# Performance work log

Measured on AMD Instinct MI355X. Metric: run time of the kernel, lower is better.

Reference implementation:

```python
import jax, jax.numpy as jnp
import numpy as np

B, S, D_IN, D_MODEL, H = 2, 2048, 1024, 1024, 16
HD = D_MODEL // H


def setup_inputs() -> dict:
    key = jax.random.key(0)
    ks = jax.random.split(key, 5)
    x = jax.random.normal(ks[0], (B, S, D_IN), dtype=jnp.float32)
    # nn.Linear default init scale ~ 1/sqrt(fan_in)
    w_qkv = jax.random.normal(ks[1], (D_IN, 3 * D_MODEL), dtype=jnp.float32) / np.sqrt(D_IN)
    b_qkv = jax.random.normal(ks[2], (3 * D_MODEL,), dtype=jnp.float32) * 0.02
    w_out = jax.random.normal(ks[3], (D_MODEL, D_MODEL), dtype=jnp.float32) / np.sqrt(D_MODEL)
    b_out = jax.random.normal(ks[4], (D_MODEL,), dtype=jnp.float32) * 0.02
    return {"x": x, "w_qkv": w_qkv, "b_qkv": b_qkv, "w_out": w_out, "b_out": b_out}


def reference(x, w_qkv, b_qkv, w_out, b_out):
    b, s, _ = x.shape
    qkv = x @ w_qkv + b_qkv                       # [b, s, 3*d_model]
    # per-head layout is [q_h | k_h | v_h]: reshape to (b, s, h, 3, hd)
    qkv = qkv.reshape(b, s, H, 3, HD).transpose(0, 2, 1, 3, 4)  # [b, h, s, 3, hd]
    q, k, v = qkv[..., 0, :], qkv[..., 1, :], qkv[..., 2, :]     # each [b, h, s, hd]
    scale = 1.0 / np.sqrt(HD).astype(np.float32)
    scores = jnp.einsum('bhqd,bhkd->bhqk', q, k) * scale         # [b, h, s, s]
    causal = jnp.tril(jnp.ones((s, s), dtype=bool))              # True = keep
    scores = jnp.where(causal, scores, -jnp.inf)
    attn = jax.nn.softmax(scores, axis=-1)
    out = jnp.einsum('bhqk,bhkd->bhqd', attn, v)                 # [b, h, s, hd]
    concat = out.transpose(0, 2, 1, 3).reshape(b, s, D_MODEL)
    return concat @ w_out + b_out
```

## Files before the change

kernel.cpp:

```cpp
#include <hip/hip_runtime.h>
#include <hip/hip_bf16.h>
#include <stdint.h>

typedef __attribute__((ext_vector_type(8))) short bf16x8;
typedef __attribute__((ext_vector_type(4))) float f32x4;

#define DEVFN static __device__ __forceinline__

typedef const __attribute__((address_space(1))) void* gas_ptr;
typedef __attribute__((address_space(3))) void* las_ptr;

DEVFN void async16(const void* g, void* l) {
  __builtin_amdgcn_global_load_lds((gas_ptr)g, (las_ptr)l, 16, 0, 0);
}

#define S_LEN 2048
#define NH    16
#define HDIM  64
#define KDIM  1024
#define NQKV  3072
#define MTOK  4096

#define QK_SCALE 0.1803368801111244f

__global__ __launch_bounds__(256) void prep_kernel(
    const float* __restrict__ x, const float* __restrict__ w_qkv,
    const float* __restrict__ w_out, __hip_bfloat16* __restrict__ xb,
    __hip_bfloat16* __restrict__ wqkt, __hip_bfloat16* __restrict__ wot) {
  __shared__ float T[64][65];
  const int j = blockIdx.x;
  const int tid = threadIdx.x;
  if (j < 2048) {
    const int i = (j * 256 + tid) * 8;
    float4 a = *(const float4*)(x + i);
    float4 b = *(const float4*)(x + i + 4);
    alignas(16) __hip_bfloat16 t[8] = {
        __float2bfloat16(a.x), __float2bfloat16(a.y),
        __float2bfloat16(a.z), __float2bfloat16(a.w),
        __float2bfloat16(b.x), __float2bfloat16(b.y),
        __float2bfloat16(b.z), __float2bfloat16(b.w)};
    *(uint4*)(xb + i) = *(const uint4*)t;
    return;
  }
  const float* in;
  __hip_bfloat16* out;
  int N, n0, k0;
  if (j < 2816) {
    const int j2 = j - 2048;
    in = w_qkv; out = wqkt; N = NQKV;
    n0 = (j2 % 48) * 64; k0 = (j2 / 48) * 64;
  } else {
    const int j3 = j - 2816;
    in = w_out; out = wot; N = KDIM;
    n0 = (j3 % 16) * 64; k0 = (j3 / 16) * 64;
  }
#pragma unroll
  for (int it = 0; it < 4; it++) {
    int r = it * 16 + (tid >> 4);
    int c = (tid & 15) * 4;
    float4 v = *(const float4*)&in[(size_t)(k0 + r) * N + n0 + c];
    T[r][c + 0] = v.x; T[r][c + 1] = v.y; T[r][c + 2] = v.z; T[r][c + 3] = v.w;
  }
  __syncthreads();
#pragma unroll
  for (int it = 0; it < 4; it++) {
    int rn = it * 16 + (tid >> 4);
    int ck = (tid & 15) * 4;
    alignas(8) __hip_bfloat16 t4[4];
#pragma unroll
    for (int jj = 0; jj < 4; jj++) t4[jj] = __float2bfloat16(T[ck + jj][rn]);
    *(ushort4*)&out[(size_t)(n0 + rn) * KDIM + k0 + ck] = *(const ushort4*)t4;
  }
}

__global__ __launch_bounds__(256, 2) void qkv_gemm_kernel(
    const __hip_bfloat16* __restrict__ A,
    const __hip_bfloat16* __restrict__ Bt,
    const float* __restrict__ bias,
    __hip_bfloat16* __restrict__ qo,
    __hip_bfloat16* __restrict__ ko,
    __hip_bfloat16* __restrict__ vto) {
  __shared__ __hip_bfloat16 As[128 * 32];
  __shared__ __hip_bfloat16 Bs[128 * 32];
  __shared__ __hip_bfloat16 Tb[4][16 * 72];
  const int tid = threadIdx.x;
  const int wave = tid >> 6, lane = tid & 63;
  const int L = lane & 15, quad = lane >> 4;
  const int wm = wave >> 1, wn = wave & 1;
  const int m0 = blockIdx.y * 128, n0 = blockIdx.x * 128;

  f32x4 acc[4][4] = {};

  const int srow = tid >> 2;
  const int scol = (tid & 3) * 8;
  const __hip_bfloat16* ag = A + (size_t)(m0 + srow) * KDIM + scol;
  const __hip_bfloat16* bg = Bt + (size_t)(n0 + srow) * KDIM + scol;
  char* asd = (char*)As + wave * 1024;
  char* bsd = (char*)Bs + wave * 1024;

  for (int kt = 0; kt < KDIM; kt += 32) {
    async16(ag + kt, asd);
    async16(ag + kt + (size_t)64 * KDIM, asd + 4096);
    async16(bg + kt, bsd);
    async16(bg + kt + (size_t)64 * KDIM, bsd + 4096);
    __syncthreads();
    bf16x8 af[4], bf[4];
#pragma unroll
    for (int r = 0; r < 4; r++)
      af[r] = *(const bf16x8*)&As[(wm * 64 + r * 16 + L) * 32 + quad * 8];
#pragma unroll
    for (int c = 0; c < 4; c++)
      bf[c] = *(const bf16x8*)&Bs[(wn * 64 + c * 16 + L) * 32 + quad * 8];
#pragma unroll
    for (int r = 0; r < 4; r++)
#pragma unroll
      for (int c = 0; c < 4; c++)
        acc[r][c] = __builtin_amdgcn_mfma_f32_16x16x32_bf16(af[r], bf[c],
                                                            acc[r][c], 0, 0, 0);
    __syncthreads();
  }

  const int mbase = m0 + wm * 64;
  const int nbase = n0 + wn * 64;
  const int h = nbase / 192;
  const int t = (nbase % 192) / 64;
  const int b = mbase >> 11;
  const int s0 = mbase & 2047;
  __hip_bfloat16* Tw = &Tb[wave][0];
  float bv[4];
#pragma unroll
  for (int c = 0; c < 4; c++) bv[c] = bias[nbase + c * 16 + L];

  if (t == 2) {
#pragma unroll
    for (int c = 0; c < 4; c++) {
#pragma unroll
      for (int r = 0; r < 4; r++) {
        alignas(8) __hip_bfloat16 t4[4];
#pragma unroll
        for (int g = 0; g < 4; g++)
          t4[g] = __float2bfloat16(acc[r][c][g] + bv[c]);
        *(ushort4*)&Tw[L * 72 + r * 16 + quad * 4] = *(const ushort4*)t4;
      }
      __asm__ volatile("s_waitcnt lgkmcnt(0)" ::: "memory");
#pragma unroll
      for (int it = 0; it < 2; it++) {
        const int rr = it * 8 + (lane >> 3);
        const int cc = (lane & 7) * 8;
        uint4 u = *(const uint4*)&Tw[rr * 72 + cc];
        *(uint4*)&vto[((size_t)((b * NH + h) * HDIM + c * 16 + rr)) * S_LEN +
                      s0 + cc] = u;
      }
    }
  } else {
    __hip_bfloat16* dst = (t == 0) ? qo : ko;
    const float sc = (t == 0) ? QK_SCALE : 1.0f;
#pragma unroll
    for (int r = 0; r < 4; r++) {
#pragma unroll
      for (int c = 0; c < 4; c++)
#pragma unroll
        for (int g = 0; g < 4; g++)
          Tw[(quad * 4 + g) * 72 + c * 16 + L] =
              __float2bfloat16((acc[r][c][g] + bv[c]) * sc);
      __asm__ volatile("s_waitcnt lgkmcnt(0)" ::: "memory");
#pragma unroll
      for (int it = 0; it < 2; it++) {
        const int rr = it * 8 + (lane >> 3);
        const int cc = (lane & 7) * 8;
        uint4 u = *(const uint4*)&Tw[rr * 72 + cc];
        *(uint4*)&dst[((size_t)((b * NH + h) * S_LEN) + s0 + r * 16 + rr) *
                          HDIM + cc] = u;
      }
    }
  }
}

__global__ __launch_bounds__(256, 2) void flash_attn_kernel(
    const __hip_bfloat16* __restrict__ q,
    const __hip_bfloat16* __restrict__ k,
    const __hip_bfloat16* __restrict__ vt,
    __hip_bfloat16* __restrict__ attn) {
  __shared__ __hip_bfloat16 Ps[4][16 * 72];
  const int tid = threadIdx.x;
  const int wave = tid >> 6, lane = tid & 63;
  const int L = lane & 15, quad = lane >> 4;

  const int j = blockIdx.x;
  const int half = j >> 8;
  const int idx = j & 255;
  const int bh = idx >> 3;
  const int p = idx & 7;
  const int qi = half ? p : (15 - p);
  const int qb = qi * 128;

  const __hip_bfloat16* Qg = q + (size_t)bh * S_LEN * HDIM;
  const __hip_bfloat16* Kg = k + (size_t)bh * S_LEN * HDIM;
  const __hip_bfloat16* Vg = vt + (size_t)bh * HDIM * S_LEN;

  int wq[2];
  wq[0] = qb + wave * 16;
  wq[1] = qb + 64 + wave * 16;

  bf16x8 qf[2][2];
#pragma unroll
  for (int r = 0; r < 2; r++)
#pragma unroll
    for (int kd = 0; kd < 2; kd++)
      qf[r][kd] =
          *(const bf16x8*)&Qg[(size_t)(wq[r] + L) * HDIM + kd * 32 + quad * 8];

  float l_i[2] = {0.f, 0.f};
  f32x4 o[2][4] = {};

  bf16x8 kc[4][2], kn[4][2];
#pragma unroll
  for (int ks = 0; ks < 4; ks++)
#pragma unroll
    for (int kd = 0; kd < 2; kd++)
      kc[ks][kd] =
          *(const bf16x8*)&Kg[(size_t)(ks * 16 + L) * HDIM + kd * 32 + quad * 8];

  const int nkt = 2 * (qi + 1);
  for (int kt = 0; kt < nkt; kt++) {
    const int k0 = kt * 64;
    bf16x8 vfr[4][2];
#pragma unroll
    for (int dsb = 0; dsb < 4; dsb++)
#pragma unroll
      for (int kf = 0; kf < 2; kf++)
        vfr[dsb][kf] = *(const bf16x8*)&Vg[(size_t)(dsb * 16 + L) * S_LEN + k0 +
                                           kf * 32 + quad * 8];

    f32x4 st[2][4] = {};
#pragma unroll
    for (int r = 0; r < 2; r++)
#pragma unroll
      for (int ks = 0; ks < 4; ks++)
#pragma unroll
        for (int kd = 0; kd < 2; kd++)
          st[r][ks] = __builtin_amdgcn_mfma_f32_16x16x32_bf16(
              kc[ks][kd], qf[r][kd], st[r][ks], 0, 0, 0);

    if (kt + 1 < nkt) {
      const int k1 = k0 + 64;
#pragma unroll
      for (int ks = 0; ks < 4; ks++)
#pragma unroll
        for (int kd = 0; kd < 2; kd++)
          kn[ks][kd] = *(const bf16x8*)&Kg[(size_t)(k1 + ks * 16 + L) * HDIM +
                                           kd * 32 + quad * 8];
    }

#pragma unroll
    for (int r = 0; r < 2; r++) {
      if (k0 > wq[r] + 15) continue;
      const int qrow = wq[r] + L;
      if (k0 + 63 > wq[r]) {
#pragma unroll
        for (int ks = 0; ks < 4; ks++)
#pragma unroll
          for (int g = 0; g < 4; g++) {
            int kk = k0 + ks * 16 + quad * 4 + g;
            if (kk > qrow) st[r][ks][g] = -1e30f;
          }
      }
      float rs = 0.f;
#pragma unroll
      for (int ks = 0; ks < 4; ks++) {
        f32x4 pv;
#pragma unroll
        for (int g = 0; g < 4; g++) {
          pv[g] = __builtin_amdgcn_exp2f(st[r][ks][g]);
          rs += pv[g];
        }
        alignas(8) __hip_bfloat16 t4[4];
#pragma unroll
        for (int g = 0; g < 4; g++) t4[g] = __float2bfloat16(pv[g]);
        *(ushort4*)&Ps[wave][L * 72 + ks * 16 + quad * 4] = *(const ushort4*)t4;
      }
      l_i[r] += rs;
      __asm__ volatile("s_waitcnt lgkmcnt(0)" ::: "memory");
      bf16x8 pf[2];
#pragma unroll
      for (int kf = 0; kf < 2; kf++)
        pf[kf] = *(const bf16x8*)&Ps[wave][L * 72 + kf * 32 + quad * 8];
#pragma unroll
      for (int dsb = 0; dsb < 4; dsb++)
#pragma unroll
        for (int kf = 0; kf < 2; kf++)
          o[r][dsb] = __builtin_amdgcn_mfma_f32_16x16x32_bf16(
              vfr[dsb][kf], pf[kf], o[r][dsb], 0, 0, 0);
    }
#pragma unroll
    for (int ks = 0; ks < 4; ks++)
#pragma unroll
      for (int kd = 0; kd < 2; kd++) kc[ks][kd] = kn[ks][kd];
  }

  const int b = bh >> 4, h = bh & 15;
#pragma unroll
  for (int r = 0; r < 2; r++) {
    float rs = l_i[r];
    rs += __shfl_xor(rs, 16, 64);
    rs += __shfl_xor(rs, 32, 64);
    const float linv = 1.0f / rs;
#pragma unroll
    for (int dsb = 0; dsb < 4; dsb++) {
      alignas(8) __hip_bfloat16 t4[4];
#pragma unroll
      for (int g = 0; g < 4; g++)
        t4[g] = __float2bfloat16(o[r][dsb][g] * linv);
      *(ushort4*)&Ps[wave][L * 72 + dsb * 16 + quad * 4] = *(const ushort4*)t4;
    }
    __asm__ volatile("s_waitcnt lgkmcnt(0)" ::: "memory");
#pragma unroll
    for (int it = 0; it < 2; it++) {
      const int row = it * 8 + (lane >> 3);
      const int col = (lane & 7) * 8;
      uint4 u = *(const uint4*)&Ps[wave][row * 72 + col];
      *(uint4*)&attn[((size_t)(b * S_LEN + wq[r] + row)) * 1024 + h * 64 + col] = u;
    }
  }
}

__global__ __launch_bounds__(256, 2) void out_gemm_kernel(
    const __hip_bfloat16* __restrict__ A,
    const __hip_bfloat16* __restrict__ Bt,
    const float* __restrict__ bias,
    float* __restrict__ out) {
  __shared__ __hip_bfloat16 As[128 * 32];
  __shared__ __hip_bfloat16 Bs[64 * 32];
  __shared__ float Os[4][16 * 36];
  const int tid = threadIdx.x;
  const int wave = tid >> 6, lane = tid & 63;
  const int L = lane & 15, quad = lane >> 4;
  const int wm = wave >> 1, wn = wave & 1;
  const int m0 = blockIdx.y * 128, n0 = blockIdx.x * 64;

  f32x4 acc[4][2] = {};

  const int srow = tid >> 2;
  const int scol = (tid & 3) * 8;
  const __hip_bfloat16* ag = A + (size_t)(m0 + srow) * KDIM + scol;
  const __hip_bfloat16* bg = Bt + (size_t)(n0 + srow) * KDIM + scol;
  char* asd = (char*)As + wave * 1024;
  char* bsd = (char*)Bs + wave * 1024;

  for (int kt = 0; kt < KDIM; kt += 32) {
    async16(ag + kt, asd);
    async16(ag + kt + (size_t)64 * KDIM, asd + 4096);
    async16(bg + kt, bsd);
    __syncthreads();
    bf16x8 af[4], bf[2];
#pragma unroll
    for (int r = 0; r < 4; r++)
      af[r] = *(const bf16x8*)&As[(wm * 64 + r * 16 + L) * 32 + quad * 8];
#pragma unroll
    for (int c = 0; c < 2; c++)
      bf[c] = *(const bf16x8*)&Bs[(wn * 32 + c * 16 + L) * 32 + quad * 8];
#pragma unroll
    for (int r = 0; r < 4; r++)
#pragma unroll
      for (int c = 0; c < 2; c++)
        acc[r][c] = __builtin_amdgcn_mfma_f32_16x16x32_bf16(af[r], bf[c],
                                                            acc[r][c], 0, 0, 0);
    __syncthreads();
  }

  float bv[2];
#pragma unroll
  for (int c = 0; c < 2; c++) bv[c] = bias[n0 + wn * 32 + c * 16 + L];
#pragma unroll
  for (int r = 0; r < 4; r++) {
#pragma unroll
    for (int c = 0; c < 2; c++)
#pragma unroll
      for (int g = 0; g < 4; g++)
        Os[wave][(quad * 4 + g) * 36 + c * 16 + L] = acc[r][c][g] + bv[c];
    __asm__ volatile("s_waitcnt lgkmcnt(0)" ::: "memory");
#pragma unroll
    for (int it = 0; it < 2; it++) {
      const int row = it * 8 + (lane >> 3);
      const int ncol = (lane & 7) * 4;
      float4 u = *(const float4*)&Os[wave][row * 36 + ncol];
      *(float4*)&out[(size_t)(m0 + wm * 64 + r * 16 + row) * 1024 + n0 +
                     wn * 32 + ncol] = u;
    }
  }
}

extern "C" void kernel_launch(void* const* d_in, const int* in_sizes, int n_in,
                              void* d_out, int out_size, void* d_ws, size_t ws_size,
                              hipStream_t stream) {
  const float* x     = (const float*)d_in[0];
  const float* w_qkv = (const float*)d_in[1];
  const float* b_qkv = (const float*)d_in[2];
  const float* w_out = (const float*)d_in[3];
  const float* b_out = (const float*)d_in[4];
  float* out = (float*)d_out;

  __hip_bfloat16* ws = (__hip_bfloat16*)d_ws;
  __hip_bfloat16* xb   = ws;
  __hip_bfloat16* wqkt = xb   + (size_t)4194304;
  __hip_bfloat16* wot  = wqkt + (size_t)3145728;
  __hip_bfloat16* qb   = wot  + (size_t)1048576;
  __hip_bfloat16* kb   = qb   + (size_t)4194304;
  __hip_bfloat16* vtb  = kb   + (size_t)4194304;
  __hip_bfloat16* attn = vtb  + (size_t)4194304;

  prep_kernel<<<3072, 256, 0, stream>>>(x, w_qkv, w_out, xb, wqkt, wot);
  qkv_gemm_kernel<<<dim3(NQKV / 128, MTOK / 128), 256, 0, stream>>>(
      xb, wqkt, b_qkv, qb, kb, vtb);
  flash_attn_kernel<<<512, 256, 0, stream>>>(qb, kb, vtb, attn);
  out_gemm_kernel<<<dim3(KDIM / 64, MTOK / 128), 256, 0, stream>>>(
      attn, wot, b_out, out);
}
```

Baseline: 200.6 us.

## Double K-step per sync in GEMMs and use 8 single-strip waves in attention

Both GEMM kernels now load two 32-wide K slices per iteration into separate LDS buffers, so each pair of barriers covers twice as many MFMAs and loop and sync overhead is halved. The flash attention kernel changes from 4 waves each handling two 16-row query strips to 8 waves each handling one strip, launched with 512 threads. Each wave also gets its own causal trip count, so waves on earlier rows stop sooner. This raises parallelism and trims masked work, but every wave now loads K and V separately, which doubles global K/V traffic per block, and LDS per GEMM block doubles.

```diff
diff --git a/kernel.cpp b/kernel.cpp
--- a/kernel.cpp
+++ b/kernel.cpp
@@ -80,8 +80,8 @@
     __hip_bfloat16* __restrict__ qo,
     __hip_bfloat16* __restrict__ ko,
     __hip_bfloat16* __restrict__ vto) {
-  __shared__ __hip_bfloat16 As[128 * 32];
-  __shared__ __hip_bfloat16 Bs[128 * 32];
+  __shared__ __hip_bfloat16 As[2][128 * 32];
+  __shared__ __hip_bfloat16 Bs[2][128 * 32];
   __shared__ __hip_bfloat16 Tb[4][16 * 72];
   const int tid = threadIdx.x;
   const int wave = tid >> 6, lane = tid & 63;
@@ -95,28 +95,41 @@
   const int scol = (tid & 3) * 8;
   const __hip_bfloat16* ag = A + (size_t)(m0 + srow) * KDIM + scol;
   const __hip_bfloat16* bg = Bt + (size_t)(n0 + srow) * KDIM + scol;
-  char* asd = (char*)As + wave * 1024;
-  char* bsd = (char*)Bs + wave * 1024;
-
-  for (int kt = 0; kt < KDIM; kt += 32) {
-    async16(ag + kt, asd);
-    async16(ag + kt + (size_t)64 * KDIM, asd + 4096);
-    async16(bg + kt, bsd);
-    async16(bg + kt + (size_t)64 * KDIM, bsd + 4096);
+  char* asd0 = (char*)&As[0][0] + wave * 1024;
+  char* asd1 = (char*)&As[1][0] + wave * 1024;
+  char* bsd0 = (char*)&Bs[0][0] + wave * 1024;
+  char* bsd1 = (char*)&Bs[1][0] + wave * 1024;
+
+  for (int kt = 0; kt < KDIM; kt += 64) {
+    async16(ag + kt, asd0);
+    async16(ag + kt + (size_t)64 * KDIM, asd0 + 4096);
+    async16(ag + kt + 32, asd1);
+    async16(ag + kt + 32 + (size_t)64 * KDIM, asd1 + 4096);
+    async16(bg + kt, bsd0);
+    async16(bg + kt + (size_t)64 * KDIM, bsd0 + 4096);
+    async16(bg + kt + 32, bsd1);
+    async16(bg + kt + 32 + (size_t)64 * KDIM, bsd1 + 4096);
     __syncthreads();
-    bf16x8 af[4], bf[4];
+    bf16x8 af[4][2], bf[4][2];
 #pragma unroll
     for (int r = 0; r < 4; r++)
-      af[r] = *(const bf16x8*)&As[(wm * 64 + r * 16 + L) * 32 + quad * 8];
+#pragma unroll
+      for (int kd = 0; kd < 2; kd++)
+        af[r][kd] = *(const bf16x8*)&As[kd][(wm * 64 + r * 16 + L) * 32 + quad * 8];
 #pragma unroll
     for (int c = 0; c < 4; c++)
-      bf[c] = *(const bf16x8*)&Bs[(wn * 64 + c * 16 + L) * 32 + quad * 8];
+#pragma unroll
+      for (int kd = 0; kd < 2; kd++)
+        bf[c][kd] = *(const bf16x8*)&Bs[kd][(wn * 64 + c * 16 + L) * 32 + quad * 8];
 #pragma unroll
     for (int r = 0; r < 4; r++)
 #pragma unroll
-      for (int c = 0; c < 4; c++)
-        acc[r][c] = __builtin_amdgcn_mfma_f32_16x16x32_bf16(af[r], bf[c],
+      for (int c = 0; c < 4; c++) {
+        acc[r][c] = __builtin_amdgcn_mfma_f32_16x16x32_bf16(af[r][0], bf[c][0],
                                                             acc[r][c], 0, 0, 0);
+        acc[r][c] = __builtin_amdgcn_mfma_f32_16x16x32_bf16(af[r][1], bf[c][1],
+                                                            acc[r][c], 0, 0, 0);
+      }
     __syncthreads();
   }
 
@@ -176,12 +189,12 @@
   }
 }
 
-__global__ __launch_bounds__(256, 2) void flash_attn_kernel(
+__global__ __launch_bounds__(512, 4) void flash_attn_kernel(
     const __hip_bfloat16* __restrict__ q,
     const __hip_bfloat16* __restrict__ k,
     const __hip_bfloat16* __restrict__ vt,
     __hip_bfloat16* __restrict__ attn) {
-  __shared__ __hip_bfloat16 Ps[4][16 * 72];
+  __shared__ __hip_bfloat16 Ps[8][16 * 72];
   const int tid = threadIdx.x;
   const int wave = tid >> 6, lane = tid & 63;
   const int L = lane & 15, quad = lane >> 4;
@@ -198,20 +211,16 @@
   const __hip_bfloat16* Kg = k + (size_t)bh * S_LEN * HDIM;
   const __hip_bfloat16* Vg = vt + (size_t)bh * HDIM * S_LEN;
 
-  int wq[2];
-  wq[0] = qb + wave * 16;
-  wq[1] = qb + 64 + wave * 16;
-
-  bf16x8 qf[2][2];
-#pragma unroll
-  for (int r = 0; r < 2; r++)
-#pragma unroll
-    for (int kd = 0; kd < 2; kd++)
-      qf[r][kd] =
-          *(const bf16x8*)&Qg[(size_t)(wq[r] + L) * HDIM + kd * 32 + quad * 8];
-
-  float l_i[2] = {0.f, 0.f};
-  f32x4 o[2][4] = {};
+  const int wq = qb + wave * 16;
+  const int qrow = wq + L;
+
+  bf16x8 qf[2];
+#pragma unroll
+  for (int kd = 0; kd < 2; kd++)
+    qf[kd] = *(const bf16x8*)&Qg[(size_t)qrow * HDIM + kd * 32 + quad * 8];
+
+  float l_i = 0.f;
+  f32x4 o[4] = {};
 
   bf16x8 kc[4][2], kn[4][2];
 #pragma unroll
@@ -221,7 +230,7 @@
       kc[ks][kd] =
           *(const bf16x8*)&Kg[(size_t)(ks * 16 + L) * HDIM + kd * 32 + quad * 8];
 
-  const int nkt = 2 * (qi + 1);
+  const int nkt = ((wq + 15) >> 6) + 1;
   for (int kt = 0; kt < nkt; kt++) {
     const int k0 = kt * 64;
     bf16x8 vfr[4][2];
@@ -232,15 +241,13 @@
         vfr[dsb][kf] = *(const bf16x8*)&Vg[(size_t)(dsb * 16 + L) * S_LEN + k0 +
                                            kf * 32 + quad * 8];
 
-    f32x4 st[2][4] = {};
-#pragma unroll
-    for (int r = 0; r < 2; r++)
-#pragma unroll
-      for (int ks = 0; ks < 4; ks++)
-#pragma unroll
-        for (int kd = 0; kd < 2; kd++)
-          st[r][ks] = __builtin_amdgcn_mfma_f32_16x16x32_bf16(
-              kc[ks][kd], qf[r][kd], st[r][ks], 0, 0, 0);
+    f32x4 st[4] = {};
+#pragma unroll
+    for (int ks = 0; ks < 4; ks++)
+#pragma unroll
+      for (int kd = 0; kd < 2; kd++)
+        st[ks] = __builtin_amdgcn_mfma_f32_16x16x32_bf16(kc[ks][kd], qf[kd],
+                                                         st[ks], 0, 0, 0);
 
     if (kt + 1 < nkt) {
       const int k1 = k0 + 64;
@@ -252,46 +259,41 @@
                                            kd * 32 + quad * 8];
     }
 
-#pragma unroll
-    for (int r = 0; r < 2; r++) {
-      if (k0 > wq[r] + 15) continue;
-      const int qrow = wq[r] + L;
-      if (k0 + 63 > wq[r]) {
-#pragma unroll
-        for (int ks = 0; ks < 4; ks++)
-#pragma unroll
-          for (int g = 0; g < 4; g++) {
-            int kk = k0 + ks * 16 + quad * 4 + g;
-            if (kk > qrow) st[r][ks][g] = -1e30f;
-          }
-      }
-      float rs = 0.f;
-#pragma unroll
-      for (int ks = 0; ks < 4; ks++) {
-        f32x4 pv;
+    if (k0 + 63 > wq) {
+#pragma unroll
+      for (int ks = 0; ks < 4; ks++)
 #pragma unroll
         for (int g = 0; g < 4; g++) {
-          pv[g] = __builtin_amdgcn_exp2f(st[r][ks][g]);
-          rs += pv[g];
+          int kk = k0 + ks * 16 + quad * 4 + g;
+          if (kk > qrow) st[ks][g] = -1e30f;
         }
-        alignas(8) __hip_bfloat16 t4[4];
-#pragma unroll
-        for (int g = 0; g < 4; g++) t4[g] = __float2bfloat16(pv[g]);
-        *(ushort4*)&Ps[wave][L * 72 + ks * 16 + quad * 4] = *(const ushort4*)t4;
-      }
-      l_i[r] += rs;
-      __asm__ volatile("s_waitcnt lgkmcnt(0)" ::: "memory");
-      bf16x8 pf[2];
+    }
+    float rs = 0.f;
+#pragma unroll
+    for (int ks = 0; ks < 4; ks++) {
+      f32x4 pv;
+#pragma unroll
+      for (int g = 0; g < 4; g++) {
+        pv[g] = __builtin_amdgcn_exp2f(st[ks][g]);
+        rs += pv[g];
+      }
+      alignas(8) __hip_bfloat16 t4[4];
+#pragma unroll
+      for (int g = 0; g < 4; g++) t4[g] = __float2bfloat16(pv[g]);
+      *(ushort4*)&Ps[wave][L * 72 + ks * 16 + quad * 4] = *(const ushort4*)t4;
+    }
+    l_i += rs;
+    __asm__ volatile("s_waitcnt lgkmcnt(0)" ::: "memory");
+    bf16x8 pf[2];
+#pragma unroll
+    for (int kf = 0; kf < 2; kf++)
+      pf[kf] = *(const bf16x8*)&Ps[wave][L * 72 + kf * 32 + quad * 8];
+#pragma unroll
+    for (int dsb = 0; dsb < 4; dsb++)
 #pragma unroll
       for (int kf = 0; kf < 2; kf++)
-        pf[kf] = *(const bf16x8*)&Ps[wave][L * 72 + kf * 32 + quad * 8];
-#pragma unroll
-      for (int dsb = 0; dsb < 4; dsb++)
-#pragma unroll
-        for (int kf = 0; kf < 2; kf++)
-          o[r][dsb] = __builtin_amdgcn_mfma_f32_16x16x32_bf16(
-              vfr[dsb][kf], pf[kf], o[r][dsb], 0, 0, 0);
-    }
+        o[dsb] = __builtin_amdgcn_mfma_f32_16x16x32_bf16(vfr[dsb][kf], pf[kf],
+                                                         o[dsb], 0, 0, 0);
 #pragma unroll
     for (int ks = 0; ks < 4; ks++)
 #pragma unroll
@@ -299,28 +301,24 @@
   }
 
   const int b = bh >> 4, h = bh & 15;
-#pragma unroll
-  for (int r = 0; r < 2; r++) {
-    float rs = l_i[r];
-    rs += __shfl_xor(rs, 16, 64);
-    rs += __shfl_xor(rs, 32, 64);
-    const float linv = 1.0f / rs;
-#pragma unroll
-    for (int dsb = 0; dsb < 4; dsb++) {
-      alignas(8) __hip_bfloat16 t4[4];
-#pragma unroll
-      for (int g = 0; g < 4; g++)
-        t4[g] = __float2bfloat16(o[r][dsb][g] * linv);
-      *(ushort4*)&Ps[wave][L * 72 + dsb * 16 + quad * 4] = *(const ushort4*)t4;
-    }
-    __asm__ volatile("s_waitcnt lgkmcnt(0)" ::: "memory");
-#pragma unroll
-    for (int it = 0; it < 2; it++) {
-      const int row = it * 8 + (lane >> 3);
-      const int col = (lane & 7) * 8;
-      uint4 u = *(const uint4*)&Ps[wave][row * 72 + col];
-      *(uint4*)&attn[((size_t)(b * S_LEN + wq[r] + row)) * 1024 + h * 64 + col] = u;
-    }
+  float rs = l_i;
+  rs += __shfl_xor(rs, 16, 64);
+  rs += __shfl_xor(rs, 32, 64);
+  const float linv = 1.0f / rs;
+#pragma unroll
+  for (int dsb = 0; dsb < 4; dsb++) {
+    alignas(8) __hip_bfloat16 t4[4];
+#pragma unroll
+    for (int g = 0; g < 4; g++) t4[g] = __float2bfloat16(o[dsb][g] * linv);
+    *(ushort4*)&Ps[wave][L * 72 + dsb * 16 + quad * 4] = *(const ushort4*)t4;
+  }
+  __asm__ volatile("s_waitcnt lgkmcnt(0)" ::: "memory");
+#pragma unroll
+  for (int it = 0; it < 2; it++) {
+    const int row = it * 8 + (lane >> 3);
+    const int col = (lane & 7) * 8;
+    uint4 u = *(const uint4*)&Ps[wave][row * 72 + col];
+    *(uint4*)&attn[((size_t)(b * S_LEN + wq + row)) * 1024 + h * 64 + col] = u;
   }
 }
 
@@ -329,8 +327,8 @@
     const __hip_bfloat16* __restrict__ Bt,
     const float* __restrict__ bias,
     float* __restrict__ out) {
-  __shared__ __hip_bfloat16 As[128 * 32];
-  __shared__ __hip_bfloat16 Bs[64 * 32];
+  __shared__ __hip_bfloat16 As[2][128 * 32];
+  __shared__ __hip_bfloat16 Bs[2][64 * 32];
   __shared__ float Os[4][16 * 36];
   const int tid = threadIdx.x;
   const int wave = tid >> 6, lane = tid & 63;
@@ -344,27 +342,39 @@
   const int scol = (tid & 3) * 8;
   const __hip_bfloat16* ag = A + (size_t)(m0 + srow) * KDIM + scol;
   const __hip_bfloat16* bg = Bt + (size_t)(n0 + srow) * KDIM + scol;
-  char* asd = (char*)As + wave * 1024;
-  char* bsd = (char*)Bs + wave * 1024;
-
-  for (int kt = 0; kt < KDIM; kt += 32) {
-    async16(ag + kt, asd);
-    async16(ag + kt + (size_t)64 * KDIM, asd + 4096);
-    async16(bg + kt, bsd);
+  char* asd0 = (char*)&As[0][0] + wave * 1024;
+  char* asd1 = (char*)&As[1][0] + wave * 1024;
+  char* bsd0 = (char*)&Bs[0][0] + wave * 1024;
+  char* bsd1 = (char*)&Bs[1][0] + wave * 1024;
+
+  for (int kt = 0; kt < KDIM; kt += 64) {
+    async16(ag + kt, asd0);
+    async16(ag + kt + (size_t)64 * KDIM, asd0 + 4096);
+    async16(ag + kt + 32, asd1);
+    async16(ag + kt + 32 + (size_t)64 * KDIM, asd1 + 4096);
+    async16(bg + kt, bsd0);
+    async16(bg + kt + 32, bsd1);
     __syncthreads();
-    bf16x8 af[4], bf[2];
+    bf16x8 af[4][2], bf[2][2];
 #pragma unroll
     for (int r = 0; r < 4; r++)
-      af[r] = *(const bf16x8*)&As[(wm * 64 + r * 16 + L) * 32 + quad * 8];
+#pragma unroll
+      for (int kd = 0; kd < 2; kd++)
+        af[r][kd] = *(const bf16x8*)&As[kd][(wm * 64 + r * 16 + L) * 32 + quad * 8];
 #pragma unroll
     for (int c = 0; c < 2; c++)
-      bf[c] = *(const bf16x8*)&Bs[(wn * 32 + c * 16 + L) * 32 + quad * 8];
+#pragma unroll
+      for (int kd = 0; kd < 2; kd++)
+        bf[c][kd] = *(const bf16x8*)&Bs[kd][(wn * 32 + c * 16 + L) * 32 + quad * 8];
 #pragma unroll
     for (int r = 0; r < 4; r++)
 #pragma unroll
-      for (int c = 0; c < 2; c++)
-        acc[r][c] = __builtin_amdgcn_mfma_f32_16x16x32_bf16(af[r], bf[c],
+      for (int c = 0; c < 2; c++) {
+        acc[r][c] = __builtin_amdgcn_mfma_f32_16x16x32_bf16(af[r][0], bf[c][0],
                                                             acc[r][c], 0, 0, 0);
+        acc[r][c] = __builtin_amdgcn_mfma_f32_16x16x32_bf16(af[r][1], bf[c][1],
+                                                            acc[r][c], 0, 0, 0);
+      }
     __syncthreads();
   }
 
@@ -412,7 +422,7 @@
   prep_kernel<<<3072, 256, 0, stream>>>(x, w_qkv, w_out, xb, wqkt, wot);
   qkv_gemm_kernel<<<dim3(NQKV / 128, MTOK / 128), 256, 0, stream>>>(
       xb, wqkt, b_qkv, qb, kb, vtb);
-  flash_attn_kernel<<<512, 256, 0, stream>>>(qb, kb, vtb, attn);
+  flash_attn_kernel<<<512, 512, 0, stream>>>(qb, kb, vtb, attn);
   out_gemm_kernel<<<dim3(KDIM / 64, MTOK / 128), 256, 0, stream>>>(
       attn, wot, b_out, out);
 }
```

Result: slower. 248.4 us (+23.8%).
